# Kernel tuning notes

Hardware: AMD Instinct MI355X
Metric: run time of the kernel (lower is better)

Reference implementation:

```python
import jax, jax.numpy as jnp
import numpy as np

N_NODES = 50000
N_EDGES = 800000
IN_DIM = 96
HID_DIM = 96


def setup_inputs() -> dict:
    key = jax.random.key(0)
    ks = jax.random.split(key, 8)
    inputs = jax.random.normal(ks[0], (N_NODES, IN_DIM), dtype=jnp.float32)
    factor = jax.random.uniform(ks[1], (N_EDGES, 1), dtype=jnp.float32)
    src = jax.random.randint(ks[2], (N_EDGES,), 0, N_NODES, dtype=jnp.int32)
    dst = jax.random.randint(ks[3], (N_EDGES,), 0, N_NODES, dtype=jnp.int32)
    # Linear params (torch nn.Linear: y = x @ W.T + b), uniform(-1/sqrt(fan_in), ..)
    s1 = 1.0 / np.sqrt(IN_DIM)
    s2 = 1.0 / np.sqrt(HID_DIM)
    W1 = jax.random.uniform(ks[4], (HID_DIM, IN_DIM), minval=-s1, maxval=s1, dtype=jnp.float32)
    b1 = jax.random.uniform(ks[5], (HID_DIM,), minval=-s1, maxval=s1, dtype=jnp.float32)
    W2 = jax.random.uniform(ks[6], (IN_DIM, HID_DIM), minval=-s2, maxval=s2, dtype=jnp.float32)
    b2 = jax.random.uniform(ks[7], (IN_DIM,), minval=-s2, maxval=s2, dtype=jnp.float32)
    return {"inputs": inputs, "W1": W1, "b1": b1, "W2": W2, "b2": b2,
            "factor": factor, "src": src, "dst": dst}


def _propagate(feat, factor, src, dst, n_nodes):
    # message = h[src] * edge_factor ; reduce = sum at dst
    msg = feat[src] * factor                       # [E, D]
    return jax.ops.segment_sum(msg, dst, num_segments=n_nodes)


def reference(inputs, W1, b1, W2, b2, factor, src, dst):
    n = inputs.shape[0]
    # in-degree norm: deg^{-1/2}, clamped at 1
    deg = jax.ops.segment_sum(jnp.ones((src.shape[0],), inputs.dtype), dst,
                              num_segments=n)
    norm = jnp.maximum(deg, 1.0) ** -0.5           # [N]
    norm = norm[:, None]                           # [N, 1]

    feat = (inputs @ W1.T + b1) * norm             # [N, H]
    h = jnp.tanh(_propagate(feat, factor, src, dst, n))

    feat = (h @ W2.T + b2) * norm                  # [N, D]
    h = jnp.tanh(_propagate(feat, factor, src, dst, n))

    # dgl.mean_nodes over a single graph -> [1, D]; unsqueeze(-1) -> [1, D, 1]
    pooled = jnp.mean(h, axis=0, keepdims=True)[..., None]
    return jnp.tanh(pooled)
```

## Files before the change

### kernel.cpp

```cpp
#include <hip/hip_runtime.h>
#include <math.h>
#include <type_traits>

#define N_NODES 50000
#define N_EDGES 800000
#define DIM 96
#define BCH 12
#define SCAN_BLK 256
#define NBLK ((N_NODES + SCAN_BLK - 1) / SCAN_BLK)
#define NPB 21
#define NBG ((N_NODES + NPB - 1) / NPB)
#define CAP 768
#define R1_ROWS 24
#define R1_BLOCKS ((NBG + R1_ROWS - 1) / R1_ROWS)

typedef short v8s __attribute__((ext_vector_type(8)));
typedef float v4f __attribute__((ext_vector_type(4)));

__device__ __forceinline__ unsigned short f2bf(float f) {
    unsigned int u = __float_as_uint(f);
    u += 0x7FFFu + ((u >> 16) & 1u);
    return (unsigned short)(u >> 16);
}
__device__ __forceinline__ unsigned int pack2bf(float lo, float hi) {
    return (unsigned int)f2bf(lo) | ((unsigned int)f2bf(hi) << 16);
}
__device__ __forceinline__ float bflo(unsigned int u) { return __uint_as_float(u << 16); }
__device__ __forceinline__ float bfhi(unsigned int u) { return __uint_as_float(u & 0xFFFF0000u); }

__device__ __forceinline__ float fast_tanh(float x) {
    float ax = fabsf(x);
    float t = __expf(-2.0f * ax);
    float r = (1.0f - t) / (1.0f + t);
    return copysignf(r, x);
}

__device__ __forceinline__ void acc8(float* a, uint4 v, float f) {
    a[0] += bflo(v.x) * f; a[1] += bfhi(v.x) * f;
    a[2] += bflo(v.y) * f; a[3] += bfhi(v.y) * f;
    a[4] += bflo(v.z) * f; a[5] += bfhi(v.z) * f;
    a[6] += bflo(v.w) * f; a[7] += bfhi(v.w) * f;
}

union U4S8 { uint4 u; v8s s; };


__global__ void count_deg(const int* __restrict__ dst, int* __restrict__ deg) {
    int e = blockIdx.x * blockDim.x + threadIdx.x;
    if (e < N_EDGES) atomicAdd(&deg[dst[e]], 1);
}

__global__ void deg_partials(const int* __restrict__ deg, float* __restrict__ norm,
                             int* __restrict__ partials) {
    int b = blockIdx.x, t = threadIdx.x;
    int n = b * SCAN_BLK + t;
    int v = 0;
    if (n < N_NODES) {
        v = deg[n];
        norm[n] = rsqrtf(fmaxf((float)v, 1.0f));
    }
    int s = v;
#pragma unroll
    for (int off = 32; off > 0; off >>= 1) s += __shfl_down(s, off, 64);
    __shared__ int ws_[4];
    if ((t & 63) == 0) ws_[t >> 6] = s;
    __syncthreads();
    if (t == 0) partials[b] = ws_[0] + ws_[1] + ws_[2] + ws_[3];
}

__global__ void scan_partials(const int* __restrict__ partials, int* __restrict__ pprefix) {
    __shared__ int sm[SCAN_BLK];
    int t = threadIdx.x;
    int v = (t < NBLK) ? partials[t] : 0;
    sm[t] = v;
    __syncthreads();
    for (int off = 1; off < SCAN_BLK; off <<= 1) {
        int u = (t >= off) ? sm[t - off] : 0;
        __syncthreads();
        sm[t] += u;
        __syncthreads();
    }
    if (t < NBLK) pprefix[t] = sm[t] - v;
}

__global__ void make_offsets(const int* __restrict__ deg, const int* __restrict__ pprefix,
                             int* __restrict__ offs, int* __restrict__ cursor) {
    __shared__ int sm[SCAN_BLK];
    int b = blockIdx.x, t = threadIdx.x;
    int idx = b * SCAN_BLK + t;
    int v = (idx < N_NODES) ? deg[idx] : 0;
    sm[t] = v;
    __syncthreads();
    for (int off = 1; off < SCAN_BLK; off <<= 1) {
        int u = (t >= off) ? sm[t - off] : 0;
        __syncthreads();
        sm[t] += u;
        __syncthreads();
    }
    if (idx < N_NODES) {
        int o = pprefix[b] + sm[t] - v;
        offs[idx] = o;
        cursor[idx] = o;
    }
    if (b == 0 && t == 0) offs[N_NODES] = N_EDGES;
}

__global__ void scatter_edges(const int* __restrict__ src, const int* __restrict__ dst,
                              const float* __restrict__ factor, int* __restrict__ cursor,
                              int2* __restrict__ entries) {
    int e = blockIdx.x * blockDim.x + threadIdx.x;
    if (e >= N_EDGES) return;
    int d = dst[e];
    int pos = atomicAdd(&cursor[d], 1);
    entries[pos] = make_int2(src[e], __float_as_int(factor[e]));
}


__global__ void swizzle_W(const float* __restrict__ W, uint4* __restrict__ bsw) {
    int idx = blockIdx.x * blockDim.x + threadIdx.x;
    if (idx >= 18 * 64) return;
    int t = idx >> 6, lane = idx & 63;
    int kt = t / 6, jt = t % 6;
    int quad = lane >> 4, l16 = lane & 15;
    const float4* wp = (const float4*)(W + (size_t)(jt * 16 + l16) * DIM + kt * 32 + quad * 8);
    float4 w0 = wp[0], w1 = wp[1];
    bsw[idx] = make_uint4(pack2bf(w0.x, w0.y), pack2bf(w0.z, w0.w),
                          pack2bf(w1.x, w1.y), pack2bf(w1.z, w1.w));
}


#define TILE_SH 104

template <typename T>
__global__ __launch_bounds__(256) void gemm_mfma(const T* __restrict__ X,
                                                 const uint4* __restrict__ bsw,
                                                 const float* __restrict__ bias,
                                                 const float* __restrict__ norm,
                                                 unsigned short* __restrict__ out) {
    __shared__ unsigned short tile[4][16 * TILE_SH];
    int tid = threadIdx.x;
    int wave = tid >> 6, lane = tid & 63;
    int quad = lane >> 4, l16 = lane & 15;
    int n0 = blockIdx.x * 64 + wave * 16;
    int rowc = min(n0 + l16, N_NODES - 1);

    uint4 bfr[18];
#pragma unroll
    for (int t = 0; t < 18; ++t) bfr[t] = bsw[t * 64 + lane];

    v4f acc[6];
#pragma unroll
    for (int jt = 0; jt < 6; ++jt) acc[jt] = (v4f)(0.0f);

#pragma unroll
    for (int kt = 0; kt < 3; ++kt) {
        U4S8 a;
        if constexpr (std::is_same_v<T, float>) {
            const float4* xp = (const float4*)(X + (size_t)rowc * DIM + kt * 32 + quad * 8);
            float4 x0 = xp[0], x1 = xp[1];
            a.u = make_uint4(pack2bf(x0.x, x0.y), pack2bf(x0.z, x0.w),
                             pack2bf(x1.x, x1.y), pack2bf(x1.z, x1.w));
        } else {
            a.u = *(const uint4*)(X + (size_t)rowc * DIM + kt * 32 + quad * 8);
        }
#pragma unroll
        for (int jt = 0; jt < 6; ++jt) {
            U4S8 bb; bb.u = bfr[kt * 6 + jt];
            acc[jt] = __builtin_amdgcn_mfma_f32_16x16x32_bf16(a.s, bb.s, acc[jt], 0, 0, 0);
        }
    }

    float nm[4];
#pragma unroll
    for (int r = 0; r < 4; ++r) nm[r] = norm[min(n0 + quad * 4 + r, N_NODES - 1)];
#pragma unroll
    for (int jt = 0; jt < 6; ++jt) {
        float bj = bias[jt * 16 + l16];
#pragma unroll
        for (int r = 0; r < 4; ++r) {
            float v = (acc[jt][r] + bj) * nm[r];
            tile[wave][(quad * 4 + r) * TILE_SH + jt * 16 + l16] = f2bf(v);
        }
    }
    __builtin_amdgcn_s_waitcnt(0);
#pragma unroll
    for (int i = 0; i < 3; ++i) {
        int chunk = lane + 64 * i;
        int rr = chunk / 12, cc = chunk - rr * 12;
        int gn = n0 + rr;
        if (gn < N_NODES) {
            uint4 v = *(uint4*)&tile[wave][rr * TILE_SH + cc * 8];
            *(uint4*)(out + (size_t)gn * DIM + cc * 8) = v;
        }
    }
}


template <bool DO_TANH, bool POOL>
__global__ void gather_agg_bf16(const unsigned short* __restrict__ feat,
                                const int* __restrict__ offs,
                                const int2* __restrict__ entries,
                                unsigned short* __restrict__ out,
                                float* __restrict__ partials) {
    __shared__ int2 ents[CAP];
    __shared__ float pool[DIM];
    __shared__ int sh_base, sh_cnt;
    int tid = threadIdx.x;
    int n0 = blockIdx.x * NPB;
    int n1 = min(n0 + NPB, N_NODES);
    if (POOL && tid < DIM) pool[tid] = 0.f;
    if (tid == 0) { sh_base = offs[n0]; sh_cnt = offs[n1] - sh_base; }
    __syncthreads();
    int base = sh_base, cnt = sh_cnt;

    int nl = tid / BCH;
    int c  = tid - nl * BCH;
    int n  = n0 + nl;
    bool active = (tid < NPB * BCH) && (n < N_NODES);
    int lb = 0, le = 0;
    if (active) { lb = offs[n] - base; le = offs[n + 1] - base; }

    float a0[8], a1[8];
#pragma unroll
    for (int i = 0; i < 8; ++i) { a0[i] = 0.f; a1[i] = 0.f; }

    for (int tb = 0; tb < cnt; tb += CAP) {
        int tcnt = min(cnt - tb, CAP);
        if (tb) __syncthreads();
        for (int i = tid; i < tcnt; i += 256) ents[i] = entries[base + tb + i];
        __syncthreads();
        int s = max(lb - tb, 0), e = min(le - tb, tcnt);
        int p = s;
        for (; p + 7 < e; p += 8) {
            int2 q0 = ents[p + 0], q1 = ents[p + 1], q2 = ents[p + 2], q3 = ents[p + 3];
            int2 q4 = ents[p + 4], q5 = ents[p + 5], q6 = ents[p + 6], q7 = ents[p + 7];
            uint4 v0 = *((const uint4*)(feat + (size_t)q0.x * DIM) + c);
            uint4 v1 = *((const uint4*)(feat + (size_t)q1.x * DIM) + c);
            uint4 v2 = *((const uint4*)(feat + (size_t)q2.x * DIM) + c);
            uint4 v3 = *((const uint4*)(feat + (size_t)q3.x * DIM) + c);
            uint4 v4 = *((const uint4*)(feat + (size_t)q4.x * DIM) + c);
            uint4 v5 = *((const uint4*)(feat + (size_t)q5.x * DIM) + c);
            uint4 v6 = *((const uint4*)(feat + (size_t)q6.x * DIM) + c);
            uint4 v7 = *((const uint4*)(feat + (size_t)q7.x * DIM) + c);
            acc8(a0, v0, __int_as_float(q0.y));
            acc8(a1, v1, __int_as_float(q1.y));
            acc8(a0, v2, __int_as_float(q2.y));
            acc8(a1, v3, __int_as_float(q3.y));
            acc8(a0, v4, __int_as_float(q4.y));
            acc8(a1, v5, __int_as_float(q5.y));
            acc8(a0, v6, __int_as_float(q6.y));
            acc8(a1, v7, __int_as_float(q7.y));
        }
        for (; p + 3 < e; p += 4) {
            int2 q0 = ents[p], q1 = ents[p + 1], q2 = ents[p + 2], q3 = ents[p + 3];
            uint4 v0 = *((const uint4*)(feat + (size_t)q0.x * DIM) + c);
            uint4 v1 = *((const uint4*)(feat + (size_t)q1.x * DIM) + c);
            uint4 v2 = *((const uint4*)(feat + (size_t)q2.x * DIM) + c);
            uint4 v3 = *((const uint4*)(feat + (size_t)q3.x * DIM) + c);
            acc8(a0, v0, __int_as_float(q0.y));
            acc8(a1, v1, __int_as_float(q1.y));
            acc8(a0, v2, __int_as_float(q2.y));
            acc8(a1, v3, __int_as_float(q3.y));
        }
        for (; p < e; ++p) {
            int2 q0 = ents[p];
            uint4 v0 = *((const uint4*)(feat + (size_t)q0.x * DIM) + c);
            acc8(a0, v0, __int_as_float(q0.y));
        }
    }

#pragma unroll
    for (int i = 0; i < 8; ++i) a0[i] += a1[i];
    if (DO_TANH || POOL) {
#pragma unroll
        for (int i = 0; i < 8; ++i) a0[i] = fast_tanh(a0[i]);
    }
    if (!POOL) {
        if (active) {
            uint4 o;
            o.x = pack2bf(a0[0], a0[1]);
            o.y = pack2bf(a0[2], a0[3]);
            o.z = pack2bf(a0[4], a0[5]);
            o.w = pack2bf(a0[6], a0[7]);
            ((uint4*)out)[n * BCH + c] = o;
        }
    } else {
        if (active) {
#pragma unroll
            for (int i = 0; i < 8; ++i) atomicAdd(&pool[c * 8 + i], a0[i]);
        }
        __syncthreads();
        if (tid < DIM) partials[(size_t)blockIdx.x * DIM + tid] = pool[tid];
    }
}


__global__ void reduce_stage1(const float* __restrict__ poolpart, float* __restrict__ stage1) {
    __shared__ float pool[DIM];
    int b = blockIdx.x, t = threadIdx.x;
    if (t < DIM) pool[t] = 0.f;
    __syncthreads();
    const int base = b * R1_ROWS * DIM;
    float loc = 0.f;
    int lastc = -1;
    for (int i = t; i < R1_ROWS * DIM; i += 256) {
        int gi = base + i;
        if (gi < NBG * DIM) {
            int col = i % DIM;
            if (col != lastc) {
                if (lastc >= 0) atomicAdd(&pool[lastc], loc);
                lastc = col; loc = 0.f;
            }
            loc += poolpart[gi];
        }
    }
    if (lastc >= 0) atomicAdd(&pool[lastc], loc);
    __syncthreads();
    if (t < DIM) stage1[b * DIM + t] = pool[t];
}

__global__ void reduce_stage2(const float* __restrict__ stage1, float* __restrict__ out) {
    __shared__ float sm[960];
    int t = threadIdx.x;
    int col = t % DIM, slice = t / DIM;
    float s = 0.f;
    for (int k = slice; k < R1_BLOCKS; k += 10) s += stage1[k * DIM + col];
    sm[t] = s;
    __syncthreads();
    if (t < DIM) {
        float tot = 0.f;
#pragma unroll
        for (int i = 0; i < 10; ++i) tot += sm[i * DIM + t];
        out[t] = tanhf(tot * (1.0f / N_NODES));
    }
}


extern "C" void kernel_launch(void* const* d_in, const int* in_sizes, int n_in,
                              void* d_out, int out_size, void* d_ws, size_t ws_size,
                              hipStream_t stream) {
    const float* inputs = (const float*)d_in[0];
    const float* W1     = (const float*)d_in[1];
    const float* b1     = (const float*)d_in[2];
    const float* W2     = (const float*)d_in[3];
    const float* b2     = (const float*)d_in[4];
    const float* factor = (const float*)d_in[5];
    const int*   src    = (const int*)d_in[6];
    const int*   dst    = (const int*)d_in[7];
    float* out = (float*)d_out;

    char* ws = (char*)d_ws;
    int*            deg      = (int*)(ws + 0);
    int*            cursor   = (int*)(ws + 262144);
    int*            offs     = (int*)(ws + 3932160);
    float*          norm     = (float*)(ws + 4194304);
    int*            partials = (int*)(ws + 4456448);
    int*            pprefix  = (int*)(ws + 4458496);
    int2*           entries  = (int2*)(ws + 4718592);
    unsigned short* bufA     = (unsigned short*)(ws + 11534336);
    unsigned short* bufB     = (unsigned short*)(ws + 21364736);
    float*          poolpart = (float*)(ws + 31195136);
    float*          stage1   = (float*)(ws + 32145536);
    uint4*          bsw1     = (uint4*)(ws + 33554432);
    uint4*          bsw2     = (uint4*)(ws + 33574912);

    swizzle_W<<<5, 256, 0, stream>>>(W1, bsw1);
    swizzle_W<<<5, 256, 0, stream>>>(W2, bsw2);

    hipMemsetAsync(deg, 0, N_NODES * sizeof(int), stream);
    count_deg<<<(N_EDGES + 255) / 256, 256, 0, stream>>>(dst, deg);
    deg_partials<<<NBLK, SCAN_BLK, 0, stream>>>(deg, norm, partials);
    scan_partials<<<1, SCAN_BLK, 0, stream>>>(partials, pprefix);
    make_offsets<<<NBLK, SCAN_BLK, 0, stream>>>(deg, pprefix, offs, cursor);
    scatter_edges<<<(N_EDGES + 255) / 256, 256, 0, stream>>>(src, dst, factor, cursor, entries);

    const int GEMM_BLOCKS = (N_NODES + 63) / 64;

    gemm_mfma<float><<<GEMM_BLOCKS, 256, 0, stream>>>(inputs, bsw1, b1, norm, bufA);
    gather_agg_bf16<true, false><<<NBG, 256, 0, stream>>>(bufA, offs, entries, bufB, nullptr);

    gemm_mfma<unsigned short><<<GEMM_BLOCKS, 256, 0, stream>>>(bufB, bsw2, b2, norm, bufA);
    gather_agg_bf16<false, true><<<NBG, 256, 0, stream>>>(bufA, offs, entries, nullptr, poolpart);

    reduce_stage1<<<R1_BLOCKS, 256, 0, stream>>>(poolpart, stage1);
    reduce_stage2<<<1, 960, 0, stream>>>(stage1, out);
}
```

Measured before the change: 271.2 us.

## Record per-edge rank in degree count and scatter CSR in destination windows

The degree-count kernel now keeps the atomicAdd return value as each edge's rank within its destination, so the scatter step computes its position as offs[d]+rank[e] and needs no second atomic pass over a cursor array. The scatter kernel also makes four passes over the edge list, each writing only edges whose destination lies in one quarter of the node range. This keeps the scattered writes inside a smaller region of memory per pass. In exchange it rereads dst four times, adds a 3.2 MB rank array to write and read, and uses a fixed grid-stride launch.

```diff
diff --git a/kernel.cpp b/kernel.cpp
--- a/kernel.cpp
+++ b/kernel.cpp
@@ -13,6 +13,8 @@
 #define CAP 768
 #define R1_ROWS 24
 #define R1_BLOCKS ((NBG + R1_ROWS - 1) / R1_ROWS)
+#define SC_PASSES 4
+#define SC_WIN ((N_NODES + SC_PASSES - 1) / SC_PASSES)
 
 typedef short v8s __attribute__((ext_vector_type(8)));
 typedef float v4f __attribute__((ext_vector_type(4)));
@@ -45,9 +47,10 @@
 union U4S8 { uint4 u; v8s s; };
 
 
-__global__ void count_deg(const int* __restrict__ dst, int* __restrict__ deg) {
+__global__ void count_deg(const int* __restrict__ dst, int* __restrict__ deg,
+                          int* __restrict__ rank) {
     int e = blockIdx.x * blockDim.x + threadIdx.x;
-    if (e < N_EDGES) atomicAdd(&deg[dst[e]], 1);
+    if (e < N_EDGES) rank[e] = atomicAdd(&deg[dst[e]], 1);
 }
 
 __global__ void deg_partials(const int* __restrict__ deg, float* __restrict__ norm,
@@ -84,7 +87,7 @@
 }
 
 __global__ void make_offsets(const int* __restrict__ deg, const int* __restrict__ pprefix,
-                             int* __restrict__ offs, int* __restrict__ cursor) {
+                             int* __restrict__ offs) {
     __shared__ int sm[SCAN_BLK];
     int b = blockIdx.x, t = threadIdx.x;
     int idx = b * SCAN_BLK + t;
@@ -97,22 +100,28 @@
         sm[t] += u;
         __syncthreads();
     }
-    if (idx < N_NODES) {
-        int o = pprefix[b] + sm[t] - v;
-        offs[idx] = o;
-        cursor[idx] = o;
-    }
+    if (idx < N_NODES) offs[idx] = pprefix[b] + sm[t] - v;
     if (b == 0 && t == 0) offs[N_NODES] = N_EDGES;
 }
 
 __global__ void scatter_edges(const int* __restrict__ src, const int* __restrict__ dst,
-                              const float* __restrict__ factor, int* __restrict__ cursor,
-                              int2* __restrict__ entries) {
-    int e = blockIdx.x * blockDim.x + threadIdx.x;
-    if (e >= N_EDGES) return;
-    int d = dst[e];
-    int pos = atomicAdd(&cursor[d], 1);
-    entries[pos] = make_int2(src[e], __float_as_int(factor[e]));
+                              const float* __restrict__ factor, const int* __restrict__ rank,
+                              const int* __restrict__ offs, int2* __restrict__ entries) {
+    int tid0 = blockIdx.x * blockDim.x + threadIdx.x;
+    int stride = gridDim.x * blockDim.x;
+#pragma unroll 1
+    for (int pass = 0; pass < SC_PASSES; ++pass) {
+        int lo = pass * SC_WIN;
+        int hi = min(lo + SC_WIN, N_NODES);
+#pragma unroll 1
+        for (int e = tid0; e < N_EDGES; e += stride) {
+            int d = dst[e];
+            if (d >= lo && d < hi) {
+                int pos = offs[d] + rank[e];
+                entries[pos] = make_int2(src[e], __float_as_int(factor[e]));
+            }
+        }
+    }
 }
 
 
@@ -351,7 +360,7 @@
 
     char* ws = (char*)d_ws;
     int*            deg      = (int*)(ws + 0);
-    int*            cursor   = (int*)(ws + 262144);
+    int*            rank     = (int*)(ws + 262144);
     int*            offs     = (int*)(ws + 3932160);
     float*          norm     = (float*)(ws + 4194304);
     int*            partials = (int*)(ws + 4456448);
@@ -368,11 +377,11 @@
     swizzle_W<<<5, 256, 0, stream>>>(W2, bsw2);
 
     hipMemsetAsync(deg, 0, N_NODES * sizeof(int), stream);
-    count_deg<<<(N_EDGES + 255) / 256, 256, 0, stream>>>(dst, deg);
+    count_deg<<<(N_EDGES + 255) / 256, 256, 0, stream>>>(dst, deg, rank);
     deg_partials<<<NBLK, SCAN_BLK, 0, stream>>>(deg, norm, partials);
     scan_partials<<<1, SCAN_BLK, 0, stream>>>(partials, pprefix);
-    make_offsets<<<NBLK, SCAN_BLK, 0, stream>>>(deg, pprefix, offs, cursor);
-    scatter_edges<<<(N_EDGES + 255) / 256, 256, 0, stream>>>(src, dst, factor, cursor, entries);
+    make_offsets<<<NBLK, SCAN_BLK, 0, stream>>>(deg, pprefix, offs);
+    scatter_edges<<<2048, 256, 0, stream>>>(src, dst, factor, rank, offs, entries);
 
     const int GEMM_BLOCKS = (N_NODES + 63) / 64;
 
```

New measurement: 237.3 us. 12.5% less time.
